# Kernel optimization log

Measured on AMD Instinct MI355X. Metric: run time of the kernel, lower is better.

## Reference

```python
import jax, jax.numpy as jnp
import numpy as np

SHAPES = ((496, 432), (248, 216), (124, 108))
NS = (40000, 20000, 8000)
T = 32
B = 4
EPS = 1e-3


def _bn(x, g, b, m, v):
    return (x - m) * (g / jnp.sqrt(v + EPS)) + b


def _vfe_scale(voxels, num_pts, w1, p1, w2, p2):
    # voxels: (N, T, 4); num_pts: (N,)
    Tp = voxels.shape[1]
    n = num_pts.astype(voxels.dtype)[:, None, None]
    m3 = voxels[:, :, :3].sum(axis=1, keepdims=True) / n
    m2 = voxels[:, :, :2].sum(axis=1, keepdims=True) / n
    feat = jnp.concatenate([voxels[:, :, :4], voxels[:, :, :3] - m3, voxels[:, :, :2] - m2], axis=-1)  # (N,T,9)
    mask = (jnp.arange(Tp)[None, :] < num_pts[:, None]).astype(voxels.dtype)[:, :, None]
    x = feat
    for w, (g, b_, rm, rv) in ((w1, p1), (w2, p2)):
        h = jax.nn.relu(_bn(jnp.einsum('ntc,cd->ntd', x, w), g, b_, rm, rv))  # (N,T,64)
        gmax = h.max(axis=1, keepdims=True)  # global max includes padded rows, as in torch source
        x = jnp.concatenate([h, jnp.broadcast_to(gmax, h.shape)], axis=-1) * mask  # (N,T,128)
    return x.max(axis=1)[:, :64]  # (N,64)


def _scatter_bev(vf, coords, h, w, batch_size):
    b = coords[:, 0]
    y = jnp.clip(coords[:, 2], 0, h - 1)
    x = jnp.clip(coords[:, 3], 0, w - 1)
    grid = jnp.zeros((batch_size, vf.shape[1], h, w), vf.dtype)
    return grid.at[b, :, y, x].set(vf)


def _fusion(x, w, g, b, m, v):
    y = jax.lax.conv_general_dilated(x, w, (1, 1), ((1, 1), (1, 1)),
                                     dimension_numbers=('NCHW', 'OIHW', 'NCHW'))
    y = _bn(y, g[None, :, None, None], b[None, :, None, None], m[None, :, None, None], v[None, :, None, None])
    return jax.nn.relu(y)


def setup_inputs() -> dict:
    key = jax.random.key(0)
    ks = jax.random.split(key, 32)
    inp = {}
    for s in range(3):
        h, w = SHAPES[s]
        inp[f'voxels_{s}'] = jax.random.normal(ks[s], (NS[s], T, 4), dtype=jnp.float32)
        inp[f'num_pts_{s}'] = jax.random.randint(ks[3 + s], (NS[s],), 1, T + 1, dtype=jnp.int32)
        b = jax.random.randint(ks[6 + s], (NS[s],), 0, B, dtype=jnp.int32)
        z = jnp.zeros((NS[s],), jnp.int32)
        y = jax.random.randint(ks[9 + s], (NS[s],), 0, h, dtype=jnp.int32)
        x = jax.random.randint(ks[12 + s], (NS[s],), 0, w, dtype=jnp.int32)
        inp[f'coords_{s}'] = jnp.stack([b, z, y, x], axis=1)
    # VFE params (stacked across the 3 scales; identical shapes per scale)
    inp['w1'] = jax.random.normal(ks[15], (3, 9, 64), dtype=jnp.float32) * 0.1
    inp['g1'] = jnp.ones((3, 64), jnp.float32) + 0.1 * jax.random.normal(ks[16], (3, 64))
    inp['b1'] = 0.05 * jax.random.normal(ks[17], (3, 64))
    inp['rm1'] = 0.05 * jax.random.normal(ks[18], (3, 64))
    inp['rv1'] = 0.5 + jnp.abs(jax.random.normal(ks[19], (3, 64)))
    inp['w2'] = jax.random.normal(ks[20], (3, 128, 64), dtype=jnp.float32) * 0.05
    inp['g2'] = jnp.ones((3, 64), jnp.float32) + 0.1 * jax.random.normal(ks[21], (3, 64))
    inp['b2'] = 0.05 * jax.random.normal(ks[22], (3, 64))
    inp['rm2'] = 0.05 * jax.random.normal(ks[23], (3, 64))
    inp['rv2'] = 0.5 + jnp.abs(jax.random.normal(ks[24], (3, 64)))
    # Fusion convs (2): Conv2d(128,64,3) + BN
    inp['fw'] = jax.random.normal(ks[25], (2, 64, 128, 3, 3), dtype=jnp.float32) * 0.03
    inp['fg'] = jnp.ones((2, 64), jnp.float32) + 0.1 * jax.random.normal(ks[26], (2, 64))
    inp['fb'] = 0.05 * jax.random.normal(ks[27], (2, 64))
    inp['fm'] = 0.05 * jax.random.normal(ks[28], (2, 64))
    inp['fv'] = 0.5 + jnp.abs(jax.random.normal(ks[29], (2, 64)))
    inp['batch_size'] = B
    return inp


def reference(voxels_0, voxels_1, voxels_2,
              w1, g1, b1, rm1, rv1, w2, g2, b2, rm2, rv2,
              fw, fg, fb, fm, fv,
              num_pts_0, num_pts_1, num_pts_2,
              coords_0, coords_1, coords_2, batch_size):
    voxels = (voxels_0, voxels_1, voxels_2)
    num_pts = (num_pts_0, num_pts_1, num_pts_2)
    coords = (coords_0, coords_1, coords_2)
    sf = []
    for s in range(3):
        vf = _vfe_scale(voxels[s], num_pts[s],
                        w1[s], (g1[s], b1[s], rm1[s], rv1[s]),
                        w2[s], (g2[s], b2[s], rm2[s], rv2[s]))
        h, w = SHAPES[s]
        sf.append(_scatter_bev(vf, coords[s], h, w, batch_size))
    # bottom-up fusion: scale2 -> scale1 -> scale0
    up = jax.image.resize(sf[2], sf[1].shape[:2] + SHAPES[1], method='bilinear')
    fused_1 = _fusion(jnp.concatenate([sf[1], up], axis=1), fw[1], fg[1], fb[1], fm[1], fv[1])
    up = jax.image.resize(fused_1, fused_1.shape[:2] + SHAPES[0], method='bilinear')
    fused_0 = _fusion(jnp.concatenate([sf[0], up], axis=1), fw[0], fg[0], fb[0], fm[0], fv[0])
    return fused_0  # spatial_features_2d: (B, 64, 496, 432)
```

## Files before the change

kernel.cpp:

```cpp
#include <hip/hip_runtime.h>

typedef unsigned short u16;
typedef short bf16x8 __attribute__((ext_vector_type(8)));
typedef float f32x4 __attribute__((ext_vector_type(4)));

#define EPSV 1e-3f

__device__ __forceinline__ float bf2f(u16 u) {
  union { unsigned int i; float f; } x; x.i = ((unsigned int)u) << 16; return x.f;
}
__device__ __forceinline__ u16 f2bf(float f) {
  union { float f; unsigned int i; } x; x.f = f;
  unsigned int r = x.i + 0x7fffu + ((x.i >> 16) & 1u);
  return (u16)(r >> 16);
}

#define WAVE_FENCE() do { __builtin_amdgcn_s_waitcnt(0); __builtin_amdgcn_wave_barrier(); } while (0)

struct VfePerWave {
  u16 X[32 * 72];
  u16 F[32 * 40];
  u16 G[64];
};
union VfeLds {
  struct { u16 W1T[64 * 40]; u16 W2T[64 * 136]; } w;
  VfePerWave r[4];
};

__device__ void vfe_body(VfeLds& lds, int lb,
    const float* __restrict__ vox, const int* __restrict__ npts,
    const float* __restrict__ w1, const float* __restrict__ g1, const float* __restrict__ b1,
    const float* __restrict__ rm1, const float* __restrict__ rv1,
    const float* __restrict__ w2, const float* __restrict__ g2, const float* __restrict__ b2,
    const float* __restrict__ rm2, const float* __restrict__ rv2,
    float* __restrict__ vf, int N)
{
  const int tid = threadIdx.x;
  const int lane = tid & 63;
  const int wv = tid >> 6;
  const int m16 = lane & 15;
  const int q = lane >> 4;

  for (int i = tid; i < 64 * 40; i += 256) {
    int c = i / 40, k = i % 40;
    lds.w.W1T[i] = f2bf(k < 9 ? w1[k * 64 + c] : 0.f);
  }
  for (int i = tid; i < 64 * 136; i += 256) {
    int c = i / 136, j = i % 136;
    lds.w.W2T[i] = f2bf(j < 128 ? w2[j * 64 + c] : 0.f);
  }
  __syncthreads();

  bf16x8 bW1[4], bLo[4][2], bHi[4][2];
  float sc1[4], sh1[4], sc2[4], sh2[4];
#pragma unroll
  for (int nf = 0; nf < 4; ++nf) {
    int c = nf * 16 + m16;
    bW1[nf] = *(const bf16x8*)&lds.w.W1T[c * 40 + q * 8];
#pragma unroll
    for (int ks = 0; ks < 2; ++ks) {
      bLo[nf][ks] = *(const bf16x8*)&lds.w.W2T[c * 136 + ks * 32 + q * 8];
      bHi[nf][ks] = *(const bf16x8*)&lds.w.W2T[c * 136 + 64 + ks * 32 + q * 8];
    }
    float s1 = g1[c] * rsqrtf(rv1[c] + EPSV);
    sc1[nf] = s1; sh1[nf] = b1[c] - rm1[c] * s1;
    float s2 = g2[c] * rsqrtf(rv2[c] + EPSV);
    sc2[nf] = s2; sh2[nf] = b2[c] - rm2[c] * s2;
  }
  __syncthreads();

  u16* X = lds.r[wv].X;
  u16* F = lds.r[wv].F;
  u16* G = lds.r[wv].G;
  for (int i = lane; i < 640; i += 64) ((unsigned int*)F)[i] = 0u;

  const int wgid = lb * 4 + wv;
  const int wstride = 4096;

  for (int v = wgid; v < N; v += wstride) {
    const int n = npts[v];
    float px = 0.f, py = 0.f, pz = 0.f, pw = 0.f;
    if (lane < 32) {
      float4 u = *(const float4*)(vox + ((size_t)v * 32 + lane) * 4);
      px = u.x; py = u.y; pz = u.z; pw = u.w;
    }
    float sx = px, sy = py, sz = pz;
#pragma unroll
    for (int off = 32; off >= 1; off >>= 1) {
      sx += __shfl_xor(sx, off);
      sy += __shfl_xor(sy, off);
      sz += __shfl_xor(sz, off);
    }
    float nf_ = (float)n;
    float mx = sx / nf_, my = sy / nf_, mz = sz / nf_;
    if (lane < 32) {
      float dx = px - mx, dy = py - my, dz = pz - mz;
      bf16x8 r0, r1;
      r0[0] = (short)f2bf(px); r0[1] = (short)f2bf(py);
      r0[2] = (short)f2bf(pz); r0[3] = (short)f2bf(pw);
      r0[4] = (short)f2bf(dx); r0[5] = (short)f2bf(dy);
      r0[6] = (short)f2bf(dz); r0[7] = (short)f2bf(dx);
      r1 = (bf16x8){0, 0, 0, 0, 0, 0, 0, 0};
      r1[0] = (short)f2bf(dy);
      *(bf16x8*)&F[lane * 40 + 0] = r0;
      *(bf16x8*)&F[lane * 40 + 8] = r1;
    }
    WAVE_FENCE();

    bf16x8 a1[2];
    a1[0] = *(const bf16x8*)&F[m16 * 40 + q * 8];
    a1[1] = *(const bf16x8*)&F[(16 + m16) * 40 + q * 8];
    f32x4 acc1[2][4];
#pragma unroll
    for (int mf = 0; mf < 2; ++mf)
#pragma unroll
      for (int nf = 0; nf < 4; ++nf) {
        acc1[mf][nf] = (f32x4){0.f, 0.f, 0.f, 0.f};
        acc1[mf][nf] = __builtin_amdgcn_mfma_f32_16x16x32_bf16(a1[mf], bW1[nf], acc1[mf][nf], 0, 0, 0);
      }

    float gmx[4] = {0.f, 0.f, 0.f, 0.f};
#pragma unroll
    for (int mf = 0; mf < 2; ++mf)
#pragma unroll
      for (int nf = 0; nf < 4; ++nf)
#pragma unroll
        for (int r = 0; r < 4; ++r) {
          float h = fmaxf(acc1[mf][nf][r] * sc1[nf] + sh1[nf], 0.f);
          gmx[nf] = fmaxf(gmx[nf], h);
          int t = mf * 16 + q * 4 + r;
          X[t * 72 + nf * 16 + m16] = f2bf(h);
        }
#pragma unroll
    for (int nf = 0; nf < 4; ++nf) {
      gmx[nf] = fmaxf(gmx[nf], __shfl_xor(gmx[nf], 16));
      gmx[nf] = fmaxf(gmx[nf], __shfl_xor(gmx[nf], 32));
    }
    if (q == 0) {
#pragma unroll
      for (int nf = 0; nf < 4; ++nf) G[nf * 16 + m16] = f2bf(gmx[nf]);
    }
    WAVE_FENCE();

    f32x4 ga[4];
#pragma unroll
    for (int nf = 0; nf < 4; ++nf) ga[nf] = (f32x4){0.f, 0.f, 0.f, 0.f};
#pragma unroll
    for (int ks = 0; ks < 2; ++ks) {
      bf16x8 ag = (bf16x8){0, 0, 0, 0, 0, 0, 0, 0};
      if (m16 == 0) ag = *(const bf16x8*)&G[ks * 32 + q * 8];
#pragma unroll
      for (int nf = 0; nf < 4; ++nf)
        ga[nf] = __builtin_amdgcn_mfma_f32_16x16x32_bf16(ag, bHi[nf][ks], ga[nf], 0, 0, 0);
    }
    float gt[4];
#pragma unroll
    for (int nf = 0; nf < 4; ++nf) {
      float s = ga[nf][0] + ga[nf][1] + ga[nf][2] + ga[nf][3];
      s += __shfl_xor(s, 16);
      s += __shfl_xor(s, 32);
      gt[nf] = s;
    }

    f32x4 acc2[2][4];
#pragma unroll
    for (int mf = 0; mf < 2; ++mf)
#pragma unroll
      for (int nf = 0; nf < 4; ++nf)
        acc2[mf][nf] = (f32x4){gt[nf], gt[nf], gt[nf], gt[nf]};
#pragma unroll
    for (int ks = 0; ks < 2; ++ks) {
      bf16x8 a2[2];
      a2[0] = *(const bf16x8*)&X[m16 * 72 + ks * 32 + q * 8];
      a2[1] = *(const bf16x8*)&X[(16 + m16) * 72 + ks * 32 + q * 8];
#pragma unroll
      for (int mf = 0; mf < 2; ++mf)
#pragma unroll
        for (int nf = 0; nf < 4; ++nf)
          acc2[mf][nf] = __builtin_amdgcn_mfma_f32_16x16x32_bf16(a2[mf], bLo[nf][ks], acc2[mf][nf], 0, 0, 0);
    }

    float vm[4] = {0.f, 0.f, 0.f, 0.f};
#pragma unroll
    for (int mf = 0; mf < 2; ++mf)
#pragma unroll
      for (int nf = 0; nf < 4; ++nf)
#pragma unroll
        for (int r = 0; r < 4; ++r) {
          int t = mf * 16 + q * 4 + r;
          float h2 = fmaxf(acc2[mf][nf][r] * sc2[nf] + sh2[nf], 0.f);
          if (t < n) vm[nf] = fmaxf(vm[nf], h2);
        }
#pragma unroll
    for (int nf = 0; nf < 4; ++nf) {
      vm[nf] = fmaxf(vm[nf], __shfl_xor(vm[nf], 16));
      vm[nf] = fmaxf(vm[nf], __shfl_xor(vm[nf], 32));
    }
    float outv = (q == 0) ? vm[0] : (q == 1) ? vm[1] : (q == 2) ? vm[2] : vm[3];
    vf[(size_t)v * 64 + q * 16 + m16] = outv;
    __builtin_amdgcn_wave_barrier();
  }
}

__global__ __launch_bounds__(256, 2) void fused1_kernel(
    const float* __restrict__ fw, u16* __restrict__ fwT,
    const float* __restrict__ vox0, const float* __restrict__ vox1, const float* __restrict__ vox2,
    const int* __restrict__ np0, const int* __restrict__ np1, const int* __restrict__ np2,
    const float* __restrict__ W1, const float* __restrict__ G1, const float* __restrict__ B1,
    const float* __restrict__ RM1, const float* __restrict__ RV1,
    const float* __restrict__ W2, const float* __restrict__ G2, const float* __restrict__ B2,
    const float* __restrict__ RM2, const float* __restrict__ RV2,
    float* __restrict__ vf0, float* __restrict__ vf1, float* __restrict__ vf2,
    const int* __restrict__ co0, const int* __restrict__ co1, const int* __restrict__ co2,
    int* __restrict__ win,
    int N0, int N1, int N2)
{
  __shared__ __align__(16) VfeLds vlds;
  int b = blockIdx.x;
  const int tid = threadIdx.x;

  if (b < 576) {
    int i = b * 256 + tid;
    int ciq = i & 31;
    int r = i >> 5;
    int co = r & 63; r >>= 6;
    int tap = r % 9; r /= 9;
    int qk = r & 3;
    int set = r >> 2;
    int ci = qk * 32 + ciq;
    fwT[i] = f2bf(fw[(((set * 64 + co) * 128 + ci) * 9) + tap]);
    return;
  }
  b -= 576;
  if (b < 3072) {
    int s = b >> 10, lb = b & 1023;
    const float* vox = (s == 0) ? vox0 : (s == 1) ? vox1 : vox2;
    const int* npts = (s == 0) ? np0 : (s == 1) ? np1 : np2;
    float* vf = (s == 0) ? vf0 : (s == 1) ? vf1 : vf2;
    int N = (s == 0) ? N0 : (s == 1) ? N1 : N2;
    vfe_body(vlds, lb, vox, npts,
             W1 + s * 576, G1 + s * 64, B1 + s * 64, RM1 + s * 64, RV1 + s * 64,
             W2 + s * 8192, G2 + s * 64, B2 + s * 64, RM2 + s * 64, RV2 + s * 64,
             vf, N);
    return;
  }
  b -= 3072;
  int t = b * 256 + tid;
  if (t >= N0 + N1 + N2) return;
  const int* coords; int H, W; int* wn; int v;
  if (t < N0)            { coords = co0; H = 496; W = 432; wn = win; v = t; }
  else if (t < N0 + N1)  { coords = co1; H = 248; W = 216; wn = win + 4 * 496 * 432; v = t - N0; }
  else                   { coords = co2; H = 124; W = 108; wn = win + 4 * 496 * 432 + 4 * 248 * 216; v = t - N0 - N1; }
  int bb = coords[v * 4 + 0];
  int y = min(max(coords[v * 4 + 2], 0), H - 1);
  int x = min(max(coords[v * 4 + 3], 0), W - 1);
  atomicMax(&wn[(bb * H + y) * W + x], v);
}

__global__ void fillf_kernel(const int* __restrict__ win,
                             const float* __restrict__ vf0, const float* __restrict__ vf1,
                             const float* __restrict__ vf2,
                             u16* __restrict__ buf0, u16* __restrict__ buf1, u16* __restrict__ g2b,
                             int c0, int c1, int c2, size_t ps0, size_t ps1) {
  int i = blockIdx.x * blockDim.x + threadIdx.x;
  if (i >= (c0 + c1 + c2) * 8) return;
  int cellg = i >> 3, c8 = (i & 7) * 8;
  int wv = win[cellg];
  const float* vf; u16* d;
  if (cellg < c0) {
    vf = vf0;
    d = buf0 + (size_t)(c8 >> 5) * ps0 + (size_t)cellg * 32 + (c8 & 31);
  } else if (cellg < c0 + c1) {
    vf = vf1;
    d = buf1 + (size_t)(c8 >> 5) * ps1 + (size_t)(cellg - c0) * 32 + (c8 & 31);
  } else {
    vf = vf2;
    d = g2b + (size_t)(cellg - c0 - c1) * 64 + c8;
  }
  bf16x8 o = (bf16x8){0, 0, 0, 0, 0, 0, 0, 0};
  if (wv >= 0) {
    const float* p = vf + (size_t)wv * 64 + c8;
    float4 v0 = *(const float4*)p;
    float4 v1 = *(const float4*)(p + 4);
    o[0] = (short)f2bf(v0.x); o[1] = (short)f2bf(v0.y);
    o[2] = (short)f2bf(v0.z); o[3] = (short)f2bf(v0.w);
    o[4] = (short)f2bf(v1.x); o[5] = (short)f2bf(v1.y);
    o[6] = (short)f2bf(v1.z); o[7] = (short)f2bf(v1.w);
  }
  *(bf16x8*)d = o;
}

__global__ void upsample_kernel(const u16* __restrict__ src, u16* __restrict__ dst,
                                int Hc, int Wc, size_t ps, int total8) {
  int i = blockIdx.x * blockDim.x + threadIdx.x;
  if (i >= total8) return;
  int c8 = (i & 7) * 8;
  int px = i >> 3;
  int W2 = Wc * 2, H2 = Hc * 2;
  int x = px % W2; int t = px / W2; int y = t % H2; int n = t / H2;
  int ky = y >> 1, kx = x >> 1;
  int ya, yb, xa, xb; float wya, wxa;
  if ((y & 1) == 0) { ya = ky > 0 ? ky - 1 : 0; yb = ky; wya = 0.25f; }
  else              { ya = ky; yb = (ky + 1 < Hc) ? ky + 1 : Hc - 1; wya = 0.75f; }
  if ((x & 1) == 0) { xa = kx > 0 ? kx - 1 : 0; xb = kx; wxa = 0.25f; }
  else              { xa = kx; xb = (kx + 1 < Wc) ? kx + 1 : Wc - 1; wxa = 0.75f; }
  float wyb = 1.f - wya, wxb = 1.f - wxa;
  const u16* sp = src + c8;
  bf16x8 vaa = *(const bf16x8*)&sp[((size_t)(n * Hc + ya) * Wc + xa) * 64];
  bf16x8 vab = *(const bf16x8*)&sp[((size_t)(n * Hc + ya) * Wc + xb) * 64];
  bf16x8 vba = *(const bf16x8*)&sp[((size_t)(n * Hc + yb) * Wc + xa) * 64];
  bf16x8 vbb = *(const bf16x8*)&sp[((size_t)(n * Hc + yb) * Wc + xb) * 64];
  bf16x8 o;
#pragma unroll
  for (int j = 0; j < 8; ++j) {
    float v = wya * (wxa * bf2f((u16)vaa[j]) + wxb * bf2f((u16)vab[j])) +
              wyb * (wxa * bf2f((u16)vba[j]) + wxb * bf2f((u16)vbb[j]));
    o[j] = (short)f2bf(v);
  }
  *(bf16x8*)&dst[(size_t)(2 + (c8 >> 5)) * ps + (size_t)px * 32 + (c8 & 31)] = o;
}

template<int H, int W, bool NCHW_OUT>
__global__ __launch_bounds__(256, 3) void conv_kernel(
    const u16* __restrict__ in, const u16* __restrict__ wT,
    const float* __restrict__ fg, const float* __restrict__ fb,
    const float* __restrict__ fm, const float* __restrict__ fv,
    void* __restrict__ outv)
{
  constexpr int XT = 32, YT = 8;
  constexpr int XTILES = (W + XT - 1) / XT;
  constexpr int YTILES = H / YT;
  constexpr int HC = XT + 2;
  constexpr int NPX = (YT + 2) * HC;
  const size_t PS = (size_t)4 * H * W * 32;
  __shared__ __align__(16) union {
    struct { char A[(NPX / 2) * 128]; char B[2][4096]; } s;
    float T[4 * 32 * 33];
  } lds;

  const int tid = threadIdx.x;
  const int lane = tid & 63;
  const int wv = tid >> 6;
  const int m16 = lane & 15;
  const int q = lane >> 4;

  int bid = blockIdx.x;
  const int xt = bid % XTILES; bid /= XTILES;
  const int yt = bid % YTILES;
  const int n = bid / YTILES;
  const int x0 = xt * XT, y0 = yt * YT;

  int lin[4];
#pragma unroll
  for (int mf = 0; mf < 4; ++mf)
    lin[mf] = (2 * wv + (mf >> 1)) * HC + ((mf & 1) << 4) + m16;

  const int bbase = ((m16 >> 1) << 7) + (((((m16 & 1) << 2) + q) ^ ((m16 >> 1) & 7)) << 4);

  f32x4 acc[4][4];
#pragma unroll
  for (int mf = 0; mf < 4; ++mf)
#pragma unroll
    for (int nf = 0; nf < 4; ++nf)
      acc[mf][nf] = (f32x4){0.f, 0.f, 0.f, 0.f};

  const int bco = tid >> 2, bs = tid & 3;
  const int bslot = ((((bco & 1) << 2) + bs) ^ ((bco >> 1) & 7));
  const int bldst = ((bco >> 1) << 7) + (bslot << 4);
  const int bgsrc = bco * 32 + bs * 8;

  for (int qk = 0; qk < 4; ++qk) {
    const u16* inq = in + (size_t)qk * PS;
    const u16* wq = wT + qk * (9 * 64 * 32);
    {
#pragma unroll
      for (int it = 0; it < 6; ++it) {
        int c = tid + it * 256;
        if (c < NPX * 4) {
          int p = c >> 2, s = c & 3;
          int r = p / HC, xx = p - r * HC;
          int gy = y0 - 1 + r, gx = x0 - 1 + xx;
          uint4 v = make_uint4(0, 0, 0, 0);
          if (gy >= 0 && gy < H && gx >= 0 && gx < W)
            v = *(const uint4*)(inq + ((size_t)((n * H + gy) * W + gx)) * 32 + s * 8);
          int slot = (((p & 1) << 2) + s) ^ ((p >> 1) & 7);
          *(uint4*)(lds.s.A + ((p >> 1) << 7) + (slot << 4)) = v;
        }
      }
      uint4 v = *(const uint4*)(wq + bgsrc);
      *(uint4*)(lds.s.B[0] + bldst) = v;
    }
    __syncthreads();

#pragma unroll
    for (int tap = 0; tap < 9; ++tap) {
      uint4 bv;
      if (tap < 8) bv = *(const uint4*)(wq + (tap + 1) * 2048 + bgsrc);
      const int tapofs = (tap / 3) * HC + (tap % 3);
      const char* Bb = lds.s.B[tap & 1];
      bf16x8 b[4], a[4];
#pragma unroll
      for (int nf = 0; nf < 4; ++nf)
        b[nf] = *(const bf16x8*)(Bb + (nf << 10) + bbase);
#pragma unroll
      for (int mf = 0; mf < 4; ++mf) {
        int hp = lin[mf] + tapofs;
        int slot = (((hp & 1) << 2) + q) ^ ((hp >> 1) & 7);
        a[mf] = *(const bf16x8*)(lds.s.A + ((hp >> 1) << 7) + (slot << 4));
      }
#pragma unroll
      for (int mf = 0; mf < 4; ++mf)
#pragma unroll
        for (int nf = 0; nf < 4; ++nf)
          acc[mf][nf] = __builtin_amdgcn_mfma_f32_16x16x32_bf16(a[mf], b[nf], acc[mf][nf], 0, 0, 0);
      if (tap < 8) *(uint4*)(lds.s.B[(tap + 1) & 1] + bldst) = bv;
      __syncthreads();
    }
  }

  float sc[4], sh[4];
#pragma unroll
  for (int nf = 0; nf < 4; ++nf) {
    int co = nf * 16 + m16;
    float s = fg[co] * rsqrtf(fv[co] + EPSV);
    sc[nf] = s;
    sh[nf] = fb[co] - fm[co] * s;
  }

  if (!NCHW_OUT) {
    u16* out = (u16*)outv;
#pragma unroll
    for (int mf = 0; mf < 4; ++mf) {
      int y = y0 + wv * 2 + (mf >> 1);
#pragma unroll
      for (int nf = 0; nf < 4; ++nf)
#pragma unroll
        for (int r = 0; r < 4; ++r) {
          int px = ((mf & 1) << 4) + q * 4 + r;
          int x = x0 + px;
          if (x < W) {
            int co = nf * 16 + m16;
            float v = fmaxf(acc[mf][nf][r] * sc[nf] + sh[nf], 0.f);
            out[((size_t)(n * H + y) * W + x) * 64 + co] = f2bf(v);
          }
        }
    }
  } else {
    __syncthreads();
    float* out = (float*)outv;
    float* T = &lds.T[wv * 32 * 33];
#pragma unroll
    for (int rr = 0; rr < 2; ++rr) {
      int y = y0 + wv * 2 + rr;
#pragma unroll
      for (int half = 0; half < 2; ++half) {
#pragma unroll
        for (int nfh = 0; nfh < 2; ++nfh) {
          int nf = half * 2 + nfh;
#pragma unroll
          for (int xc = 0; xc < 2; ++xc) {
            int mf = rr * 2 + xc;
#pragma unroll
            for (int r = 0; r < 4; ++r) {
              int px = (xc << 4) + q * 4 + r;
              int col = nfh * 16 + m16;
              T[col * 33 + px] = fmaxf(acc[mf][nf][r] * sc[nf] + sh[nf], 0.f);
            }
          }
        }
        WAVE_FENCE();
        const int px = lane & 31, co2 = lane >> 5;
        int x = x0 + px;
#pragma unroll 4
        for (int it = 0; it < 16; ++it) {
          int col = it * 2 + co2;
          int co = half * 32 + col;
          float v = T[col * 33 + px];
          if (x < W) out[((size_t)(n * 64 + co) * H + y) * W + x] = v;
        }
        WAVE_FENCE();
      }
    }
  }
}

extern "C" void kernel_launch(void* const* d_in, const int* in_sizes, int n_in,
                              void* d_out, int out_size, void* d_ws, size_t ws_size,
                              hipStream_t stream) {
  int I_vox[3], I_np[3], I_co[3];
  int I_w1, I_g1, I_b1, I_rm1, I_rv1, I_w2, I_g2, I_b2, I_rm2, I_rv2;
  int I_fw, I_fg, I_fb, I_fm, I_fv;
  if (in_sizes[1] == 40000) {
    I_vox[0] = 0; I_np[0] = 1; I_co[0] = 2;
    I_vox[1] = 3; I_np[1] = 4; I_co[1] = 5;
    I_vox[2] = 6; I_np[2] = 7; I_co[2] = 8;
    I_w1 = 9; I_g1 = 10; I_b1 = 11; I_rm1 = 12; I_rv1 = 13;
    I_w2 = 14; I_g2 = 15; I_b2 = 16; I_rm2 = 17; I_rv2 = 18;
    I_fw = 19; I_fg = 20; I_fb = 21; I_fm = 22; I_fv = 23;
  } else {
    I_vox[0] = 0; I_vox[1] = 1; I_vox[2] = 2;
    I_w1 = 3; I_g1 = 4; I_b1 = 5; I_rm1 = 6; I_rv1 = 7;
    I_w2 = 8; I_g2 = 9; I_b2 = 10; I_rm2 = 11; I_rv2 = 12;
    I_fw = 13; I_fg = 14; I_fb = 15; I_fm = 16; I_fv = 17;
    I_np[0] = 18; I_np[1] = 19; I_np[2] = 20;
    I_co[0] = 21; I_co[1] = 22; I_co[2] = 23;
  }

  const int HS[3] = {496, 248, 124};
  const int WS[3] = {432, 216, 108};
  int Nv[3];
  for (int s = 0; s < 3; ++s) Nv[s] = in_sizes[I_np[s]];

  char* wsp = (char*)d_ws;
  size_t off = 0;
  auto take = [&](size_t bytes) -> void* {
    void* p = wsp + off;
    off = (off + bytes + 255) & ~(size_t)255;
    return p;
  };
  float* vf[3];
  for (int s = 0; s < 3; ++s) vf[s] = (float*)take((size_t)Nv[s] * 64 * 4);
  int cells[3];
  for (int s = 0; s < 3; ++s) cells[s] = 4 * HS[s] * WS[s];
  int cellsTot = cells[0] + cells[1] + cells[2];
  int* win = (int*)take((size_t)cellsTot * 4);
  u16* buf0 = (u16*)take((size_t)cells[0] * 128 * 2);
  u16* buf1 = (u16*)take((size_t)cells[1] * 128 * 2);
  u16* g2b  = (u16*)take((size_t)cells[2] * 64 * 2);
  u16* fus1 = (u16*)take((size_t)cells[1] * 64 * 2);
  u16* fwT  = (u16*)take((size_t)2 * 4 * 9 * 64 * 32 * 2);

  const float* W1 = (const float*)d_in[I_w1];
  const float* G1 = (const float*)d_in[I_g1];
  const float* B1 = (const float*)d_in[I_b1];
  const float* RM1 = (const float*)d_in[I_rm1];
  const float* RV1 = (const float*)d_in[I_rv1];
  const float* W2 = (const float*)d_in[I_w2];
  const float* G2 = (const float*)d_in[I_g2];
  const float* B2 = (const float*)d_in[I_b2];
  const float* RM2 = (const float*)d_in[I_rm2];
  const float* RV2 = (const float*)d_in[I_rv2];
  const float* FW = (const float*)d_in[I_fw];
  const float* FG = (const float*)d_in[I_fg];
  const float* FB = (const float*)d_in[I_fb];
  const float* FM = (const float*)d_in[I_fm];
  const float* FV = (const float*)d_in[I_fv];

  hipMemsetAsync(win, 0xFF, (size_t)cellsTot * 4, stream);

  {
    int winB = (Nv[0] + Nv[1] + Nv[2] + 255) / 256;
    fused1_kernel<<<576 + 3072 + winB, 256, 0, stream>>>(
        FW, fwT,
        (const float*)d_in[I_vox[0]], (const float*)d_in[I_vox[1]], (const float*)d_in[I_vox[2]],
        (const int*)d_in[I_np[0]], (const int*)d_in[I_np[1]], (const int*)d_in[I_np[2]],
        W1, G1, B1, RM1, RV1, W2, G2, B2, RM2, RV2,
        vf[0], vf[1], vf[2],
        (const int*)d_in[I_co[0]], (const int*)d_in[I_co[1]], (const int*)d_in[I_co[2]],
        win, Nv[0], Nv[1], Nv[2]);
  }

  const size_t ps0 = (size_t)cells[0] * 32;
  const size_t ps1 = (size_t)cells[1] * 32;
  fillf_kernel<<<(cellsTot * 8 + 255) / 256, 256, 0, stream>>>(
      win, vf[0], vf[1], vf[2], buf0, buf1, g2b, cells[0], cells[1], cells[2], ps0, ps1);

  {
    int total8 = cells[1] * 8;
    upsample_kernel<<<(total8 + 255) / 256, 256, 0, stream>>>(g2b, buf1, 124, 108, ps1, total8);
  }
  conv_kernel<248, 216, false><<<4 * (248 / 8) * 7, 256, 0, stream>>>(
      buf1, fwT + 4 * 9 * 64 * 32, FG + 64, FB + 64, FM + 64, FV + 64, fus1);
  {
    int total8 = cells[0] * 8;
    upsample_kernel<<<(total8 + 255) / 256, 256, 0, stream>>>(fus1, buf0, 248, 216, ps0, total8);
  }
  conv_kernel<496, 432, true><<<4 * (496 / 8) * 14, 256, 0, stream>>>(
      buf0, fwT, FG, FB, FM, FV, (float*)d_out);
}
```

Before: 711.2 us.

## Fuse BEV scatter gather into conv input loading, drop dense scatter buffers

The scatter-fill pass that wrote dense bf16 BEV grids for scales 0 and 1 is removed. The conv kernels now look up the winner index per pixel for the first two channel quarters and read the voxel features directly, converting them to bf16 during the LDS tile load. Only scale 2 is still materialized for upsampling, and the concat buffers shrink to hold just the upsampled half. This saves a large write plus re-read of dense grids, at the cost of an indirect gather and conversion inside the conv load, which is re-done for halo pixels shared by neighbouring tiles.

```diff
diff --git a/kernel.cpp b/kernel.cpp
--- a/kernel.cpp
+++ b/kernel.cpp
@@ -257,29 +257,15 @@
   atomicMax(&wn[(bb * H + y) * W + x], v);
 }
 
-__global__ void fillf_kernel(const int* __restrict__ win,
-                             const float* __restrict__ vf0, const float* __restrict__ vf1,
-                             const float* __restrict__ vf2,
-                             u16* __restrict__ buf0, u16* __restrict__ buf1, u16* __restrict__ g2b,
-                             int c0, int c1, int c2, size_t ps0, size_t ps1) {
+__global__ void fill2_kernel(const int* __restrict__ win2, const float* __restrict__ vf2,
+                             u16* __restrict__ g2b, int cells2) {
   int i = blockIdx.x * blockDim.x + threadIdx.x;
-  if (i >= (c0 + c1 + c2) * 8) return;
-  int cellg = i >> 3, c8 = (i & 7) * 8;
-  int wv = win[cellg];
-  const float* vf; u16* d;
-  if (cellg < c0) {
-    vf = vf0;
-    d = buf0 + (size_t)(c8 >> 5) * ps0 + (size_t)cellg * 32 + (c8 & 31);
-  } else if (cellg < c0 + c1) {
-    vf = vf1;
-    d = buf1 + (size_t)(c8 >> 5) * ps1 + (size_t)(cellg - c0) * 32 + (c8 & 31);
-  } else {
-    vf = vf2;
-    d = g2b + (size_t)(cellg - c0 - c1) * 64 + c8;
-  }
+  if (i >= cells2 * 8) return;
+  int cell = i >> 3, c8 = (i & 7) * 8;
+  int wv = win2[cell];
   bf16x8 o = (bf16x8){0, 0, 0, 0, 0, 0, 0, 0};
   if (wv >= 0) {
-    const float* p = vf + (size_t)wv * 64 + c8;
+    const float* p = vf2 + (size_t)wv * 64 + c8;
     float4 v0 = *(const float4*)p;
     float4 v1 = *(const float4*)(p + 4);
     o[0] = (short)f2bf(v0.x); o[1] = (short)f2bf(v0.y);
@@ -287,7 +273,7 @@
     o[4] = (short)f2bf(v1.x); o[5] = (short)f2bf(v1.y);
     o[6] = (short)f2bf(v1.z); o[7] = (short)f2bf(v1.w);
   }
-  *(bf16x8*)d = o;
+  *(bf16x8*)&g2b[(size_t)cell * 64 + c8] = o;
 }
 
 __global__ void upsample_kernel(const u16* __restrict__ src, u16* __restrict__ dst,
@@ -317,12 +303,13 @@
               wyb * (wxa * bf2f((u16)vba[j]) + wxb * bf2f((u16)vbb[j]));
     o[j] = (short)f2bf(v);
   }
-  *(bf16x8*)&dst[(size_t)(2 + (c8 >> 5)) * ps + (size_t)px * 32 + (c8 & 31)] = o;
+  *(bf16x8*)&dst[(size_t)(c8 >> 5) * ps + (size_t)px * 32 + (c8 & 31)] = o;
 }
 
 template<int H, int W, bool NCHW_OUT>
 __global__ __launch_bounds__(256, 3) void conv_kernel(
-    const u16* __restrict__ in, const u16* __restrict__ wT,
+    const u16* __restrict__ in, const int* __restrict__ win,
+    const float* __restrict__ vfp, const u16* __restrict__ wT,
     const float* __restrict__ fg, const float* __restrict__ fb,
     const float* __restrict__ fm, const float* __restrict__ fv,
     void* __restrict__ outv)
@@ -370,7 +357,6 @@
   const int bgsrc = bco * 32 + bs * 8;
 
   for (int qk = 0; qk < 4; ++qk) {
-    const u16* inq = in + (size_t)qk * PS;
     const u16* wq = wT + qk * (9 * 64 * 32);
     {
 #pragma unroll
@@ -381,8 +367,23 @@
           int r = p / HC, xx = p - r * HC;
           int gy = y0 - 1 + r, gx = x0 - 1 + xx;
           uint4 v = make_uint4(0, 0, 0, 0);
-          if (gy >= 0 && gy < H && gx >= 0 && gx < W)
-            v = *(const uint4*)(inq + ((size_t)((n * H + gy) * W + gx)) * 32 + s * 8);
+          if (gy >= 0 && gy < H && gx >= 0 && gx < W) {
+            size_t pix = (size_t)((n * H + gy) * W + gx);
+            if (qk < 2) {
+              int wvx = win[pix];
+              if (wvx >= 0) {
+                const float* pf = vfp + (size_t)wvx * 64 + qk * 32 + s * 8;
+                float4 f0 = *(const float4*)pf;
+                float4 f1 = *(const float4*)(pf + 4);
+                v.x = (unsigned)f2bf(f0.x) | ((unsigned)f2bf(f0.y) << 16);
+                v.y = (unsigned)f2bf(f0.z) | ((unsigned)f2bf(f0.w) << 16);
+                v.z = (unsigned)f2bf(f1.x) | ((unsigned)f2bf(f1.y) << 16);
+                v.w = (unsigned)f2bf(f1.z) | ((unsigned)f2bf(f1.w) << 16);
+              }
+            } else {
+              v = *(const uint4*)(in + (size_t)(qk - 2) * PS + pix * 32 + s * 8);
+            }
+          }
           int slot = (((p & 1) << 2) + s) ^ ((p >> 1) & 7);
           *(uint4*)(lds.s.A + ((p >> 1) << 7) + (slot << 4)) = v;
         }
@@ -524,8 +525,8 @@
   for (int s = 0; s < 3; ++s) cells[s] = 4 * HS[s] * WS[s];
   int cellsTot = cells[0] + cells[1] + cells[2];
   int* win = (int*)take((size_t)cellsTot * 4);
-  u16* buf0 = (u16*)take((size_t)cells[0] * 128 * 2);
-  u16* buf1 = (u16*)take((size_t)cells[1] * 128 * 2);
+  u16* buf0 = (u16*)take((size_t)cells[0] * 64 * 2);
+  u16* buf1 = (u16*)take((size_t)cells[1] * 64 * 2);
   u16* g2b  = (u16*)take((size_t)cells[2] * 64 * 2);
   u16* fus1 = (u16*)take((size_t)cells[1] * 64 * 2);
   u16* fwT  = (u16*)take((size_t)2 * 4 * 9 * 64 * 32 * 2);
@@ -560,21 +561,22 @@
         win, Nv[0], Nv[1], Nv[2]);
   }
 
+  int* win1 = win + cells[0];
+  int* win2 = win + cells[0] + cells[1];
+  fill2_kernel<<<(cells[2] * 8 + 255) / 256, 256, 0, stream>>>(win2, vf[2], g2b, cells[2]);
+
   const size_t ps0 = (size_t)cells[0] * 32;
   const size_t ps1 = (size_t)cells[1] * 32;
-  fillf_kernel<<<(cellsTot * 8 + 255) / 256, 256, 0, stream>>>(
-      win, vf[0], vf[1], vf[2], buf0, buf1, g2b, cells[0], cells[1], cells[2], ps0, ps1);
-
   {
     int total8 = cells[1] * 8;
     upsample_kernel<<<(total8 + 255) / 256, 256, 0, stream>>>(g2b, buf1, 124, 108, ps1, total8);
   }
   conv_kernel<248, 216, false><<<4 * (248 / 8) * 7, 256, 0, stream>>>(
-      buf1, fwT + 4 * 9 * 64 * 32, FG + 64, FB + 64, FM + 64, FV + 64, fus1);
+      buf1, win1, vf[1], fwT + 4 * 9 * 64 * 32, FG + 64, FB + 64, FM + 64, FV + 64, fus1);
   {
     int total8 = cells[0] * 8;
     upsample_kernel<<<(total8 + 255) / 256, 256, 0, stream>>>(fus1, buf0, 248, 216, ps0, total8);
   }
   conv_kernel<496, 432, true><<<4 * (496 / 8) * 14, 256, 0, stream>>>(
-      buf0, fwT, FG, FB, FM, FV, (float*)d_out);
-}
+      buf0, win, vf[0], fwT, FG, FB, FM, FV, (float*)d_out);
+}
```

Measured after the change: 795.9 us. +11.9%, slower.
